# Kernel tuning notes

Measured on AMD Instinct MI355X. Metric: run time of the kernel, lower is better.

The kernel has to match this reference:

```python
import jax, jax.numpy as jnp
import numpy as np

NEG_BIG = -9e15
ALPHA = 0.2  # LeakyReLU negative slope


def setup_inputs() -> dict:
    key = jax.random.key(0)
    k1, k2, k3, k4 = jax.random.split(key, 4)
    N, F_in, F_out = 10000, 512, 64
    inp = {
        "input": jax.random.normal(k1, (N, F_in), dtype=jnp.float32),
        "W": jax.random.normal(k2, (F_in, F_out), dtype=jnp.float32) * (1.414 / np.sqrt(F_in)),
        "a": jax.random.normal(k3, (2 * F_out, 1), dtype=jnp.float32) * 0.1,
        "adj": jax.random.randint(k4, (N, N), 0, 2, dtype=jnp.int32),
    }
    return inp


def reference(input, W, a, adj):
    # h: [N, F'] projected features
    h = input @ W
    F_out = h.shape[1]
    # e_ij = LeakyReLU([h_i || h_j] . a) == LeakyReLU(h@a1 + (h@a2)^T)
    # (mathematically identical, avoids materializing [N, N, 2F'])
    a1, a2 = a[:F_out], a[F_out:]          # each [F', 1]
    e = (h @ a1) + (h @ a2).T              # [N, N]
    e = jax.nn.leaky_relu(e, negative_slope=ALPHA)
    # adjacency-masked softmax over neighbors j
    e = jnp.where(adj > 0, e, NEG_BIG)
    attention = jax.nn.softmax(e, axis=1)  # [N, N]
    # weighted aggregation
    h_prime = attention @ h                # [N, F']
    # concat=True -> ELU activation
    return jax.nn.elu(h_prime)
```

## Files before the change

### kernel.cpp

```cpp
#include <hip/hip_runtime.h>
#include <hip/hip_bf16.h>

#define N_NODES 10000
#define FIN 512
#define FOUT 64
#define NP 10016
#define LEAKY_ALPHA 0.2f
#define TOTAL_STEPS 313

typedef __attribute__((ext_vector_type(8))) short short8;
typedef __attribute__((ext_vector_type(4))) float f32x4;
typedef __attribute__((ext_vector_type(8))) __bf16 bf16x8;

static __device__ __forceinline__ unsigned short f2bf(float f) {
  unsigned u = __builtin_bit_cast(unsigned, f);
  u += 0x7FFFu + ((u >> 16) & 1u);
  return (unsigned short)(u >> 16);
}
static __device__ __forceinline__ float bf2f(unsigned short s) {
  unsigned u = ((unsigned)s) << 16;
  return __builtin_bit_cast(float, u);
}
static __device__ __forceinline__ unsigned enc_f32(float f) {
  unsigned u = __builtin_bit_cast(unsigned, f);
  return (u & 0x80000000u) ? ~u : (u | 0x80000000u);
}
static __device__ __forceinline__ float dec_f32(unsigned u) {
  unsigned b = (u & 0x80000000u) ? (u & 0x7FFFFFFFu) : ~u;
  return __builtin_bit_cast(float, b);
}

__global__ __launch_bounds__(64) void gat_h(
    const float* __restrict__ input, const float* __restrict__ W,
    const float* __restrict__ a, float* __restrict__ s1,
    float* __restrict__ s2, unsigned short* __restrict__ hbT,
    unsigned int* __restrict__ maxbits) {
  __shared__ float in_lds[8 * FIN];
  const int l = threadIdx.x;
  const int rb = blockIdx.x * 8;

  const float4* src = (const float4*)(input + (size_t)rb * FIN);
  float4* dst = (float4*)in_lds;
#pragma unroll
  for (int v = 0; v < 16; ++v) dst[l + 64 * v] = src[l + 64 * v];
  __syncthreads();

  float acc[8] = {0.f, 0.f, 0.f, 0.f, 0.f, 0.f, 0.f, 0.f};
  for (int k4 = 0; k4 < FIN / 4; ++k4) {
    float w0 = W[(k4 * 4 + 0) * FOUT + l];
    float w1 = W[(k4 * 4 + 1) * FOUT + l];
    float w2 = W[(k4 * 4 + 2) * FOUT + l];
    float w3 = W[(k4 * 4 + 3) * FOUT + l];
#pragma unroll
    for (int r = 0; r < 8; ++r) {
      float4 iv = *(const float4*)&in_lds[r * FIN + k4 * 4];
      acc[r] = fmaf(iv.x, w0, fmaf(iv.y, w1, fmaf(iv.z, w2, fmaf(iv.w, w3, acc[r]))));
    }
  }

  short8 pk;
#pragma unroll
  for (int r = 0; r < 8; ++r) pk[r] = (short)f2bf(acc[r]);
  *(short8*)(hbT + (size_t)l * NP + rb) = pk;

  const float a1l = a[l], a2l = a[FOUT + l];
  float m1 = -1e30f, m2 = -1e30f;
#pragma unroll
  for (int r = 0; r < 8; ++r) {
    float v1 = acc[r] * a1l, v2 = acc[r] * a2l;
#pragma unroll
    for (int off = 32; off > 0; off >>= 1) {
      v1 += __shfl_xor(v1, off);
      v2 += __shfl_xor(v2, off);
    }
    if (l == 0) { s1[rb + r] = v1; s2[rb + r] = v2; }
    m1 = fmaxf(m1, v1);
    m2 = fmaxf(m2, v2);
  }
  if (l == 0) {
    atomicMax(maxbits + 0, enc_f32(m1));
    atomicMax(maxbits + 1, enc_f32(m2));
  }
}

__global__ __launch_bounds__(64) void gat_attn(
    const int* __restrict__ adj, const float* __restrict__ s1,
    const float* __restrict__ s2, const unsigned short* __restrict__ hbT,
    const unsigned int* __restrict__ maxbits,
    float* __restrict__ num_part, float* __restrict__ den_part,
    int steps_per_chunk) {
  const int l = threadIdx.x;
  const int r = l & 15;
  const int g = l >> 4;
  const int kb = g * 8;
  const int row_base = blockIdx.x * 16;
  const int split = blockIdx.y;

  const float msum = dec_f32(maxbits[0]) + dec_f32(maxbits[1]);
  const float m = (msum > 0.f) ? msum : LEAKY_ALPHA * msum;

  int sb = split * steps_per_chunk;
  int se = sb + steps_per_chunk;
  if (se > TOTAL_STEPS) se = TOTAL_STEPS;
  bool has_tail = false;
  if (se == TOTAL_STEPS) { has_tail = true; se = TOTAL_STEPS - 1; }

  const float s1r = s1[row_base + r];
  const int* __restrict__ adjp = adj + (size_t)(row_base + r) * N_NODES;
  const unsigned short* __restrict__ bp = hbT + (size_t)r * NP;

  f32x4 acc0 = {0.f, 0.f, 0.f, 0.f};
  f32x4 acc1 = {0.f, 0.f, 0.f, 0.f};
  f32x4 acc2 = {0.f, 0.f, 0.f, 0.f};
  f32x4 acc3 = {0.f, 0.f, 0.f, 0.f};
  float den_acc = 0.f;

  for (int t = sb; t < se; ++t) {
    const int j = t * 32 + kb;
    int4 av0 = *(const int4*)(adjp + j);
    int4 av1 = *(const int4*)(adjp + j + 4);
    float4 sv0 = *(const float4*)(s2 + j);
    float4 sv1 = *(const float4*)(s2 + j + 4);
    short8 b0 = *(const short8*)(bp + j);
    short8 b1 = *(const short8*)(bp + 16 * NP + j);
    short8 b2 = *(const short8*)(bp + 32 * NP + j);
    short8 b3 = *(const short8*)(bp + 48 * NP + j);

    float sef[8] = {sv0.x, sv0.y, sv0.z, sv0.w, sv1.x, sv1.y, sv1.z, sv1.w};
    int ad[8] = {av0.x, av0.y, av0.z, av0.w, av1.x, av1.y, av1.z, av1.w};
    short8 af;
#pragma unroll
    for (int e = 0; e < 8; ++e) {
      float ee = s1r + sef[e];
      ee = (ee >= 0.f) ? ee : LEAKY_ALPHA * ee;
      float w = (ad[e] > 0) ? __expf(ee - m) : 0.f;
      unsigned short wb = f2bf(w);
      af[e] = (short)wb;
      den_acc += bf2f(wb);
    }
    bf16x8 av = __builtin_bit_cast(bf16x8, af);
    acc0 = __builtin_amdgcn_mfma_f32_16x16x32_bf16(av, __builtin_bit_cast(bf16x8, b0), acc0, 0, 0, 0);
    acc1 = __builtin_amdgcn_mfma_f32_16x16x32_bf16(av, __builtin_bit_cast(bf16x8, b1), acc1, 0, 0, 0);
    acc2 = __builtin_amdgcn_mfma_f32_16x16x32_bf16(av, __builtin_bit_cast(bf16x8, b2), acc2, 0, 0, 0);
    acc3 = __builtin_amdgcn_mfma_f32_16x16x32_bf16(av, __builtin_bit_cast(bf16x8, b3), acc3, 0, 0, 0);
  }

  if (has_tail) {
    short8 af = {0, 0, 0, 0, 0, 0, 0, 0};
    short8 b0 = {0, 0, 0, 0, 0, 0, 0, 0};
    short8 b1 = {0, 0, 0, 0, 0, 0, 0, 0};
    short8 b2 = {0, 0, 0, 0, 0, 0, 0, 0};
    short8 b3 = {0, 0, 0, 0, 0, 0, 0, 0};
    if (g < 2) {
      const int j = 9984 + kb;
      int4 av0 = *(const int4*)(adjp + j);
      int4 av1 = *(const int4*)(adjp + j + 4);
      float4 sv0 = *(const float4*)(s2 + j);
      float4 sv1 = *(const float4*)(s2 + j + 4);
      b0 = *(const short8*)(bp + j);
      b1 = *(const short8*)(bp + 16 * NP + j);
      b2 = *(const short8*)(bp + 32 * NP + j);
      b3 = *(const short8*)(bp + 48 * NP + j);
      float sef[8] = {sv0.x, sv0.y, sv0.z, sv0.w, sv1.x, sv1.y, sv1.z, sv1.w};
      int ad[8] = {av0.x, av0.y, av0.z, av0.w, av1.x, av1.y, av1.z, av1.w};
#pragma unroll
      for (int e = 0; e < 8; ++e) {
        float ee = s1r + sef[e];
        ee = (ee >= 0.f) ? ee : LEAKY_ALPHA * ee;
        float w = (ad[e] > 0) ? __expf(ee - m) : 0.f;
        unsigned short wb = f2bf(w);
        af[e] = (short)wb;
        den_acc += bf2f(wb);
      }
    }
    bf16x8 av = __builtin_bit_cast(bf16x8, af);
    acc0 = __builtin_amdgcn_mfma_f32_16x16x32_bf16(av, __builtin_bit_cast(bf16x8, b0), acc0, 0, 0, 0);
    acc1 = __builtin_amdgcn_mfma_f32_16x16x32_bf16(av, __builtin_bit_cast(bf16x8, b1), acc1, 0, 0, 0);
    acc2 = __builtin_amdgcn_mfma_f32_16x16x32_bf16(av, __builtin_bit_cast(bf16x8, b2), acc2, 0, 0, 0);
    acc3 = __builtin_amdgcn_mfma_f32_16x16x32_bf16(av, __builtin_bit_cast(bf16x8, b3), acc3, 0, 0, 0);
  }

  den_acc += __shfl_xor(den_acc, 16);
  den_acc += __shfl_xor(den_acc, 32);
  if (l < 16) den_part[(size_t)split * N_NODES + row_base + r] = den_acc;

  float* np_ = num_part + ((size_t)split * N_NODES + row_base) * FOUT;
#pragma unroll
  for (int q = 0; q < 4; ++q) {
    const int orow = g * 4 + q;
    np_[orow * FOUT + 0 + r] = acc0[q];
    np_[orow * FOUT + 16 + r] = acc1[q];
    np_[orow * FOUT + 32 + r] = acc2[q];
    np_[orow * FOUT + 48 + r] = acc3[q];
  }
}

__global__ __launch_bounds__(256) void gat_out(
    const float* __restrict__ num_part, const float* __restrict__ den_part,
    const unsigned short* __restrict__ hbT, float* __restrict__ out, int S) {
  const int idx = blockIdx.x * 256 + threadIdx.x;
  if (idx >= N_NODES * FOUT) return;
  const int i = idx >> 6, f = idx & 63;
  float den = 0.f, num = 0.f;
  for (int s = 0; s < S; ++s) {
    den += den_part[(size_t)s * N_NODES + i];
    num += num_part[(size_t)s * N_NODES * FOUT + idx];
  }
  float v;
  if (den > 0.f) {
    v = num / den;
  } else {
    float sum = 0.f;
    for (int j = 0; j < N_NODES; ++j) sum += bf2f(hbT[(size_t)f * NP + j]);
    v = sum / (float)N_NODES;
  }
  out[idx] = (v > 0.f) ? v : (__expf(v) - 1.f);
}

extern "C" void kernel_launch(void* const* d_in, const int* in_sizes, int n_in,
                              void* d_out, int out_size, void* d_ws, size_t ws_size,
                              hipStream_t stream) {
  const float* input = (const float*)d_in[0];
  const float* W = (const float*)d_in[1];
  const float* a = (const float*)d_in[2];
  const int* adj = (const int*)d_in[3];
  float* out = (float*)d_out;

  int S = 4;
  {
    size_t need4 = (size_t)4 * N_NODES * FOUT * 4 + (size_t)4 * N_NODES * 4 + 64 +
                   (size_t)N_NODES * 4 + (size_t)NP * 4 + (size_t)FOUT * NP * 2 + 256;
    if (ws_size < need4) S = 1;
  }

  char* p = (char*)d_ws;
  float* num_part = (float*)p;               p += (size_t)S * N_NODES * FOUT * 4;
  float* den_part = (float*)p;               p += (size_t)S * N_NODES * 4;
  unsigned int* maxbits = (unsigned int*)p;  p += 64;
  float* s1 = (float*)p;                     p += (size_t)N_NODES * 4;
  float* s2 = (float*)p;                     p += (size_t)NP * 4;
  unsigned short* hbT = (unsigned short*)p;

  size_t zero_bytes = (size_t)S * N_NODES * FOUT * 4 + (size_t)S * N_NODES * 4 + 8;
  hipMemsetAsync(d_ws, 0, zero_bytes, stream);

  hipLaunchKernelGGL(gat_h, dim3(N_NODES / 8), dim3(64), 0, stream,
                     input, W, a, s1, s2, hbT, maxbits);

  int steps_per_chunk = (TOTAL_STEPS + S - 1) / S;
  hipLaunchKernelGGL(gat_attn, dim3(N_NODES / 16, S), dim3(64), 0, stream,
                     adj, s1, s2, hbT, maxbits, num_part, den_part, steps_per_chunk);

  hipLaunchKernelGGL(gat_out, dim3((N_NODES * FOUT + 255) / 256), dim3(256), 0, stream,
                     num_part, den_part, hbT, out, S);
}
```

Baseline: 684.7 us.

## Software-pipeline attention loads, compute denominators via MFMA, raise split count

The attention loop is now double-buffered, issuing the next step's adjacency, s2 and hbT loads before the current step's compute. The softmax denominator is produced by an extra MFMA against a ones vector instead of per-element scalar adds. Mask and LeakyReLU become branchless (multiply by adj, fmaxf). The K split count rises from 4 to 8 to add parallelism. Workspace is reordered so only the max bits are memset rather than the large partial buffers, which relies on every partial slot being fully written; in exchange there is one more MFMA per step and more register pressure.

```diff
diff --git a/kernel.cpp b/kernel.cpp
--- a/kernel.cpp
+++ b/kernel.cpp
@@ -5,12 +5,12 @@
 #define FIN 512
 #define FOUT 64
 #define NP 10016
-#define LEAKY_ALPHA 0.2f
 #define TOTAL_STEPS 313
 
 typedef __attribute__((ext_vector_type(8))) short short8;
 typedef __attribute__((ext_vector_type(4))) float f32x4;
 typedef __attribute__((ext_vector_type(8))) __bf16 bf16x8;
+typedef __attribute__((ext_vector_type(4))) unsigned int uint4v;
 
 static __device__ __forceinline__ unsigned short f2bf(float f) {
   unsigned u = __builtin_bit_cast(unsigned, f);
@@ -28,6 +28,16 @@
 static __device__ __forceinline__ float dec_f32(unsigned u) {
   unsigned b = (u & 0x80000000u) ? (u & 0x7FFFFFFFu) : ~u;
   return __builtin_bit_cast(float, b);
+}
+
+static __device__ __forceinline__ unsigned wpair(float s1r, float sA, float sB,
+                                                 int adA, int adB, float m) {
+  float eA = s1r + sA, eB = s1r + sB;
+  eA = fmaxf(eA, 0.2f * eA);
+  eB = fmaxf(eB, 0.2f * eB);
+  float wA = __expf(eA - m) * (float)adA;
+  float wB = __expf(eB - m) * (float)adB;
+  return ((unsigned)f2bf(wB) << 16) | (unsigned)f2bf(wA);
 }
 
 __global__ __launch_bounds__(64) void gat_h(
@@ -97,7 +107,7 @@
   const int split = blockIdx.y;
 
   const float msum = dec_f32(maxbits[0]) + dec_f32(maxbits[1]);
-  const float m = (msum > 0.f) ? msum : LEAKY_ALPHA * msum;
+  const float m = fmaxf(msum, 0.2f * msum);
 
   int sb = split * steps_per_chunk;
   int se = sb + steps_per_chunk;
@@ -109,80 +119,99 @@
   const int* __restrict__ adjp = adj + (size_t)(row_base + r) * N_NODES;
   const unsigned short* __restrict__ bp = hbT + (size_t)r * NP;
 
+  short8 ones_s;
+#pragma unroll
+  for (int e = 0; e < 8; ++e) ones_s[e] = (short)0x3F80;
+  const bf16x8 onesv = __builtin_bit_cast(bf16x8, ones_s);
+
   f32x4 acc0 = {0.f, 0.f, 0.f, 0.f};
   f32x4 acc1 = {0.f, 0.f, 0.f, 0.f};
   f32x4 acc2 = {0.f, 0.f, 0.f, 0.f};
   f32x4 acc3 = {0.f, 0.f, 0.f, 0.f};
-  float den_acc = 0.f;
-
-  for (int t = sb; t < se; ++t) {
-    const int j = t * 32 + kb;
-    int4 av0 = *(const int4*)(adjp + j);
-    int4 av1 = *(const int4*)(adjp + j + 4);
-    float4 sv0 = *(const float4*)(s2 + j);
-    float4 sv1 = *(const float4*)(s2 + j + 4);
-    short8 b0 = *(const short8*)(bp + j);
-    short8 b1 = *(const short8*)(bp + 16 * NP + j);
-    short8 b2 = *(const short8*)(bp + 32 * NP + j);
-    short8 b3 = *(const short8*)(bp + 48 * NP + j);
-
-    float sef[8] = {sv0.x, sv0.y, sv0.z, sv0.w, sv1.x, sv1.y, sv1.z, sv1.w};
-    int ad[8] = {av0.x, av0.y, av0.z, av0.w, av1.x, av1.y, av1.z, av1.w};
-    short8 af;
-#pragma unroll
-    for (int e = 0; e < 8; ++e) {
-      float ee = s1r + sef[e];
-      ee = (ee >= 0.f) ? ee : LEAKY_ALPHA * ee;
-      float w = (ad[e] > 0) ? __expf(ee - m) : 0.f;
-      unsigned short wb = f2bf(w);
-      af[e] = (short)wb;
-      den_acc += bf2f(wb);
-    }
-    bf16x8 av = __builtin_bit_cast(bf16x8, af);
-    acc0 = __builtin_amdgcn_mfma_f32_16x16x32_bf16(av, __builtin_bit_cast(bf16x8, b0), acc0, 0, 0, 0);
-    acc1 = __builtin_amdgcn_mfma_f32_16x16x32_bf16(av, __builtin_bit_cast(bf16x8, b1), acc1, 0, 0, 0);
-    acc2 = __builtin_amdgcn_mfma_f32_16x16x32_bf16(av, __builtin_bit_cast(bf16x8, b2), acc2, 0, 0, 0);
-    acc3 = __builtin_amdgcn_mfma_f32_16x16x32_bf16(av, __builtin_bit_cast(bf16x8, b3), acc3, 0, 0, 0);
+  f32x4 accd = {0.f, 0.f, 0.f, 0.f};
+
+#define LOADS(T, a0_, a1_, s0_, s1_, b0_, b1_, b2_, b3_) do {                \
+    const int jj_ = (T) * 32 + kb;                                           \
+    a0_ = *(const int4*)(adjp + jj_);                                        \
+    a1_ = *(const int4*)(adjp + jj_ + 4);                                    \
+    s0_ = *(const float4*)(s2 + jj_);                                        \
+    s1_ = *(const float4*)(s2 + jj_ + 4);                                    \
+    b0_ = *(const short8*)(bp + jj_);                                        \
+    b1_ = *(const short8*)(bp + 16 * NP + jj_);                              \
+    b2_ = *(const short8*)(bp + 32 * NP + jj_);                              \
+    b3_ = *(const short8*)(bp + 48 * NP + jj_);                              \
+  } while (0)
+
+#define STEPC(a0_, a1_, s0_, s1_, b0_, b1_, b2_, b3_) do {                   \
+    uint4v au_;                                                              \
+    au_.x = wpair(s1r, s0_.x, s0_.y, a0_.x, a0_.y, m);                       \
+    au_.y = wpair(s1r, s0_.z, s0_.w, a0_.z, a0_.w, m);                       \
+    au_.z = wpair(s1r, s1_.x, s1_.y, a1_.x, a1_.y, m);                       \
+    au_.w = wpair(s1r, s1_.z, s1_.w, a1_.z, a1_.w, m);                       \
+    bf16x8 av_ = __builtin_bit_cast(bf16x8, au_);                            \
+    acc0 = __builtin_amdgcn_mfma_f32_16x16x32_bf16(av_, __builtin_bit_cast(bf16x8, b0_), acc0, 0, 0, 0); \
+    acc1 = __builtin_amdgcn_mfma_f32_16x16x32_bf16(av_, __builtin_bit_cast(bf16x8, b1_), acc1, 0, 0, 0); \
+    acc2 = __builtin_amdgcn_mfma_f32_16x16x32_bf16(av_, __builtin_bit_cast(bf16x8, b2_), acc2, 0, 0, 0); \
+    acc3 = __builtin_amdgcn_mfma_f32_16x16x32_bf16(av_, __builtin_bit_cast(bf16x8, b3_), acc3, 0, 0, 0); \
+    accd = __builtin_amdgcn_mfma_f32_16x16x32_bf16(av_, onesv, accd, 0, 0, 0); \
+  } while (0)
+
+  int4 Aa0, Aa1; float4 As0, As1; short8 Ab0, Ab1, Ab2, Ab3;
+  int4 Ba0, Ba1; float4 Bs0, Bs1; short8 Bb0, Bb1, Bb2, Bb3;
+
+  int t = sb;
+  if (se > sb) {
+    LOADS(t, Aa0, Aa1, As0, As1, Ab0, Ab1, Ab2, Ab3);
+    for (; t + 2 < se; t += 2) {
+      LOADS(t + 1, Ba0, Ba1, Bs0, Bs1, Bb0, Bb1, Bb2, Bb3);
+      STEPC(Aa0, Aa1, As0, As1, Ab0, Ab1, Ab2, Ab3);
+      LOADS(t + 2, Aa0, Aa1, As0, As1, Ab0, Ab1, Ab2, Ab3);
+      STEPC(Ba0, Ba1, Bs0, Bs1, Bb0, Bb1, Bb2, Bb3);
+    }
+    if (se - t == 2) {
+      LOADS(t + 1, Ba0, Ba1, Bs0, Bs1, Bb0, Bb1, Bb2, Bb3);
+      STEPC(Aa0, Aa1, As0, As1, Ab0, Ab1, Ab2, Ab3);
+      STEPC(Ba0, Ba1, Bs0, Bs1, Bb0, Bb1, Bb2, Bb3);
+    } else {
+      STEPC(Aa0, Aa1, As0, As1, Ab0, Ab1, Ab2, Ab3);
+    }
   }
 
   if (has_tail) {
-    short8 af = {0, 0, 0, 0, 0, 0, 0, 0};
-    short8 b0 = {0, 0, 0, 0, 0, 0, 0, 0};
-    short8 b1 = {0, 0, 0, 0, 0, 0, 0, 0};
-    short8 b2 = {0, 0, 0, 0, 0, 0, 0, 0};
-    short8 b3 = {0, 0, 0, 0, 0, 0, 0, 0};
+    uint4v au_ = {0u, 0u, 0u, 0u};
+    short8 tb0 = {0,0,0,0,0,0,0,0}, tb1 = {0,0,0,0,0,0,0,0};
+    short8 tb2 = {0,0,0,0,0,0,0,0}, tb3 = {0,0,0,0,0,0,0,0};
     if (g < 2) {
-      const int j = 9984 + kb;
-      int4 av0 = *(const int4*)(adjp + j);
-      int4 av1 = *(const int4*)(adjp + j + 4);
-      float4 sv0 = *(const float4*)(s2 + j);
-      float4 sv1 = *(const float4*)(s2 + j + 4);
-      b0 = *(const short8*)(bp + j);
-      b1 = *(const short8*)(bp + 16 * NP + j);
-      b2 = *(const short8*)(bp + 32 * NP + j);
-      b3 = *(const short8*)(bp + 48 * NP + j);
-      float sef[8] = {sv0.x, sv0.y, sv0.z, sv0.w, sv1.x, sv1.y, sv1.z, sv1.w};
-      int ad[8] = {av0.x, av0.y, av0.z, av0.w, av1.x, av1.y, av1.z, av1.w};
-#pragma unroll
-      for (int e = 0; e < 8; ++e) {
-        float ee = s1r + sef[e];
-        ee = (ee >= 0.f) ? ee : LEAKY_ALPHA * ee;
-        float w = (ad[e] > 0) ? __expf(ee - m) : 0.f;
-        unsigned short wb = f2bf(w);
-        af[e] = (short)wb;
-        den_acc += bf2f(wb);
-      }
-    }
-    bf16x8 av = __builtin_bit_cast(bf16x8, af);
-    acc0 = __builtin_amdgcn_mfma_f32_16x16x32_bf16(av, __builtin_bit_cast(bf16x8, b0), acc0, 0, 0, 0);
-    acc1 = __builtin_amdgcn_mfma_f32_16x16x32_bf16(av, __builtin_bit_cast(bf16x8, b1), acc1, 0, 0, 0);
-    acc2 = __builtin_amdgcn_mfma_f32_16x16x32_bf16(av, __builtin_bit_cast(bf16x8, b2), acc2, 0, 0, 0);
-    acc3 = __builtin_amdgcn_mfma_f32_16x16x32_bf16(av, __builtin_bit_cast(bf16x8, b3), acc3, 0, 0, 0);
-  }
-
-  den_acc += __shfl_xor(den_acc, 16);
-  den_acc += __shfl_xor(den_acc, 32);
-  if (l < 16) den_part[(size_t)split * N_NODES + row_base + r] = den_acc;
+      const int jj_ = 9984 + kb;
+      int4 ta0 = *(const int4*)(adjp + jj_);
+      int4 ta1 = *(const int4*)(adjp + jj_ + 4);
+      float4 ts0 = *(const float4*)(s2 + jj_);
+      float4 ts1 = *(const float4*)(s2 + jj_ + 4);
+      tb0 = *(const short8*)(bp + jj_);
+      tb1 = *(const short8*)(bp + 16 * NP + jj_);
+      tb2 = *(const short8*)(bp + 32 * NP + jj_);
+      tb3 = *(const short8*)(bp + 48 * NP + jj_);
+      au_.x = wpair(s1r, ts0.x, ts0.y, ta0.x, ta0.y, m);
+      au_.y = wpair(s1r, ts0.z, ts0.w, ta0.z, ta0.w, m);
+      au_.z = wpair(s1r, ts1.x, ts1.y, ta1.x, ta1.y, m);
+      au_.w = wpair(s1r, ts1.z, ts1.w, ta1.z, ta1.w, m);
+    }
+    bf16x8 av_ = __builtin_bit_cast(bf16x8, au_);
+    acc0 = __builtin_amdgcn_mfma_f32_16x16x32_bf16(av_, __builtin_bit_cast(bf16x8, tb0), acc0, 0, 0, 0);
+    acc1 = __builtin_amdgcn_mfma_f32_16x16x32_bf16(av_, __builtin_bit_cast(bf16x8, tb1), acc1, 0, 0, 0);
+    acc2 = __builtin_amdgcn_mfma_f32_16x16x32_bf16(av_, __builtin_bit_cast(bf16x8, tb2), acc2, 0, 0, 0);
+    acc3 = __builtin_amdgcn_mfma_f32_16x16x32_bf16(av_, __builtin_bit_cast(bf16x8, tb3), acc3, 0, 0, 0);
+    accd = __builtin_amdgcn_mfma_f32_16x16x32_bf16(av_, onesv, accd, 0, 0, 0);
+  }
+
+#undef LOADS
+#undef STEPC
+
+  if (r == 0) {
+#pragma unroll
+    for (int q = 0; q < 4; ++q)
+      den_part[(size_t)split * N_NODES + row_base + g * 4 + q] = accd[q];
+  }
 
   float* np_ = num_part + ((size_t)split * N_NODES + row_base) * FOUT;
 #pragma unroll
@@ -226,23 +255,20 @@
   const int* adj = (const int*)d_in[3];
   float* out = (float*)d_out;
 
-  int S = 4;
-  {
-    size_t need4 = (size_t)4 * N_NODES * FOUT * 4 + (size_t)4 * N_NODES * 4 + 64 +
-                   (size_t)N_NODES * 4 + (size_t)NP * 4 + (size_t)FOUT * NP * 2 + 256;
-    if (ws_size < need4) S = 1;
-  }
+  const size_t fixed = 64 + (size_t)N_NODES * 4 + (size_t)NP * 4 + (size_t)FOUT * NP * 2 + 256;
+  int S = 8;
+  if (ws_size < fixed + (size_t)8 * N_NODES * (FOUT * 4 + 4)) S = 4;
+  if (ws_size < fixed + (size_t)4 * N_NODES * (FOUT * 4 + 4)) S = 1;
 
   char* p = (char*)d_ws;
-  float* num_part = (float*)p;               p += (size_t)S * N_NODES * FOUT * 4;
-  float* den_part = (float*)p;               p += (size_t)S * N_NODES * 4;
   unsigned int* maxbits = (unsigned int*)p;  p += 64;
   float* s1 = (float*)p;                     p += (size_t)N_NODES * 4;
   float* s2 = (float*)p;                     p += (size_t)NP * 4;
-  unsigned short* hbT = (unsigned short*)p;
-
-  size_t zero_bytes = (size_t)S * N_NODES * FOUT * 4 + (size_t)S * N_NODES * 4 + 8;
-  hipMemsetAsync(d_ws, 0, zero_bytes, stream);
+  unsigned short* hbT = (unsigned short*)p;  p += (size_t)FOUT * NP * 2;
+  float* num_part = (float*)p;               p += (size_t)S * N_NODES * FOUT * 4;
+  float* den_part = (float*)p;
+
+  (void)hipMemsetAsync(maxbits, 0, 8, stream);
 
   hipLaunchKernelGGL(gat_h, dim3(N_NODES / 8), dim3(64), 0, stream,
                      input, W, a, s1, s2, hbT, maxbits);
```

Result: no change. 676.5 us (-1.2%).
